# Performance work log

Hardware: AMD Instinct MI355X
Metric: run time of the kernel (lower is better)

## Reference

```python
import jax, jax.numpy as jnp
import numpy as np

B, T, DMODEL = 2, 2048, 1024
H, DK, DV = 16, 64, 64
FF = 4096
EPS = 1e-5


def _layernorm_2d(x):
    # torch LayerNorm(normalized_shape=(T, dmodel)): normalize jointly over last two
    # dims, biased variance, weight=1 / bias=0 (freshly constructed each forward).
    mu = jnp.mean(x, axis=(1, 2), keepdims=True)
    var = jnp.mean((x - mu) ** 2, axis=(1, 2), keepdims=True)
    return (x - mu) / jnp.sqrt(var + EPS)


def setup_inputs() -> dict:
    key = jax.random.key(0)
    ks = jax.random.split(key, 9)
    s = 0.02  # small init for numerical sanity (original uses uniform(-1,1))
    return {
        "x": jax.random.normal(ks[0], (B, T, DMODEL), jnp.float32),
        "Wq": jax.random.normal(ks[1], (H, DMODEL, DK), jnp.float32) * s,
        "Wk": jax.random.normal(ks[2], (H, DMODEL, DK), jnp.float32) * s,
        "Wv": jax.random.normal(ks[3], (H, DMODEL, DV), jnp.float32) * s,
        "Wo": jax.random.normal(ks[4], (DMODEL, DMODEL), jnp.float32) * s,
        "W1": jax.random.normal(ks[5], (DMODEL, FF), jnp.float32) * s,
        "b1": jnp.zeros((FF,), jnp.float32),
        "W2": jax.random.normal(ks[6], (FF, DMODEL), jnp.float32) * s,
        "b2": jnp.zeros((DMODEL,), jnp.float32),
    }


def reference(x, Wq, Wk, Wv, Wo, W1, b1, W2, b2):
    b, t, d = x.shape
    h, _, dk = Wq.shape
    dv = Wv.shape[-1]
    # per-head projections: (B,H,T,dk/dv)
    Qp = jnp.einsum("btd,hdk->bhtk", x, Wq)
    Kp = jnp.einsum("btd,hdk->bhtk", x, Wk)
    Vp = jnp.einsum("btd,hdv->bhtv", x, Wv)
    scores = jnp.einsum("bhqk,bhsk->bhqs", Qp, Kp) / np.sqrt(dk).astype(np.float32)
    # NOTE: original does torch.softmax(heads, 2) -> softmax over the QUERY axis
    attn = jax.nn.softmax(scores, axis=2)
    heads = jnp.einsum("bhqs,bhsv->bqhv", attn, Vp).reshape(b, t, h * dv)
    att_out = heads @ Wo
    o1 = _layernorm_2d(x + att_out)
    ff = jnp.maximum(o1 @ W1 + b1, 0.0) @ W2 + b2
    return _layernorm_2d(o1 + ff)
```

## Files before the change

### kernel.cpp

```cpp
#include <hip/hip_runtime.h>
#include <hip/hip_bf16.h>
#include <cstddef>
#include <cstdint>

typedef __hip_bfloat16 hbf;
typedef __attribute__((ext_vector_type(8))) __bf16 bf16x8;
typedef __attribute__((ext_vector_type(4))) float f32x4;

#define B_ 2
#define T_ 2048
#define D_ 1024
#define H_ 16
#define FF_ 4096
#define EPS_ 1e-5f
#define SCALE_ 0.125f

__device__ __forceinline__ float bf2f(hbf v) { return __bfloat162float(v); }
__device__ __forceinline__ float ldin(const void* p, size_t i, int isbf) {
  return isbf ? __bfloat162float(((const hbf*)p)[i]) : ((const float*)p)[i];
}
__device__ __forceinline__ void ston(void* p, size_t i, float v, int isbf) {
  if (isbf) ((hbf*)p)[i] = __float2bfloat16(v);
  else ((float*)p)[i] = v;
}
__device__ __forceinline__ f32x4 mfma16(bf16x8 a, bf16x8 b, f32x4 c) {
  return __builtin_amdgcn_mfma_f32_16x16x32_bf16(a, b, c, 0, 0, 0);
}
__device__ __forceinline__ bf16x8 ldfrag(const hbf* p) {
  return *(const bf16x8*)p;
}
__device__ __forceinline__ void glds16(const hbf* g, hbf* l) {
  __builtin_amdgcn_global_load_lds(
      (const __attribute__((address_space(1))) void*)g,
      (__attribute__((address_space(3))) void*)l, 16, 0, 0);
}

__global__ __launch_bounds__(256) void detect_dtype(const unsigned* x,
                                                    int* flag) {
  __shared__ int cnt[256];
  int c = 0;
  for (int i = threadIdx.x; i < 4096; i += 256) {
    unsigned low = x[i] & 0xFFFFu;
    unsigned e = (low >> 7) & 0xFFu;
    if (e >= 100u && e <= 142u) c++;
  }
  cnt[threadIdx.x] = c;
  __syncthreads();
  for (int off = 128; off > 0; off >>= 1) {
    if ((int)threadIdx.x < off) cnt[threadIdx.x] += cnt[threadIdx.x + off];
    __syncthreads();
  }
  if (threadIdx.x == 0) *flag = (cnt[0] > 2458) ? 1 : 0;
}

__global__ __launch_bounds__(256) void cvt_copy(const void* __restrict__ src,
                                                hbf* __restrict__ dst, size_t n,
                                                const int* __restrict__ flag) {
  const int f = *flag;
  for (size_t i = (size_t)blockIdx.x * 256 + threadIdx.x; i < n;
       i += (size_t)gridDim.x * 256) {
    dst[i] = __float2bfloat16(ldin(src, i, f));
  }
}

__global__ __launch_bounds__(256) void tr_k(const void* __restrict__ src,
                                            hbf* __restrict__ dst, int R, int C,
                                            const int* __restrict__ flag) {
  __shared__ float tile[32][33];
  const int f = *flag;
  const int z = blockIdx.z;
  const int c0 = blockIdx.x * 32, r0 = blockIdx.y * 32;
  const int tx = threadIdx.x & 31, ty = threadIdx.x >> 5;
  const size_t base = (size_t)z * R * C;
#pragma unroll
  for (int p = 0; p < 4; p++) {
    int rr = p * 8 + ty;
    tile[rr][tx] = ldin(src, base + (size_t)(r0 + rr) * C + c0 + tx, f);
  }
  __syncthreads();
#pragma unroll
  for (int p = 0; p < 4; p++) {
    int cc = p * 8 + ty;
    dst[base + (size_t)(c0 + cc) * R + r0 + tx] = __float2bfloat16(tile[tx][cc]);
  }
}

__global__ __launch_bounds__(256) void vt_k(const hbf* __restrict__ V,
                                            const float* __restrict__ coladj,
                                            hbf* __restrict__ Vt) {
  __shared__ hbf tile[64][72];
  const int bh = blockIdx.y;
  const int t0 = blockIdx.x * 64;
  const int tid = threadIdx.x;
  const hbf* Vb = V + (size_t)bh * T_ * 64;
  const float* adjb = coladj + (size_t)bh * T_;
  hbf* Vtb = Vt + (size_t)bh * 64 * T_;
#pragma unroll
  for (int c = 0; c < 2; c++) {
    int e = (c * 256 + tid) * 8;
    int r = e >> 6, col = e & 63;
    union alignas(16) {
      hbf h[8];
      float4 f4;
    } u;
    u.f4 = *(const float4*)(&Vb[(size_t)(t0 + r) * 64 + col]);
    float sc = __expf(-adjb[t0 + r]);
#pragma unroll
    for (int k2 = 0; k2 < 8; k2++)
      u.h[k2] = __float2bfloat16(bf2f(u.h[k2]) * sc);
    *(float4*)(&tile[r][col]) = u.f4;
  }
  __syncthreads();
#pragma unroll
  for (int c = 0; c < 2; c++) {
    int e = (c * 256 + tid) * 8;
    int v = e >> 6, tt = e & 63;
    union alignas(16) {
      hbf h[8];
      float4 f4;
    } u;
#pragma unroll
    for (int k2 = 0; k2 < 8; k2++) u.h[k2] = tile[tt + k2][v];
    *(float4*)(&Vtb[(size_t)v * T_ + t0 + tt]) = u.f4;
  }
}

template <int MODE, int BM, int BN>
__global__ __launch_bounds__(256) void gemm_bt(
    const hbf* __restrict__ A, const hbf* __restrict__ Bt, hbf* __restrict__ C,
    const hbf* __restrict__ e1, const hbf* __restrict__ e2, int M, int N,
    int K) {
  constexpr int WM = BM / 2, WN = BN / 2;
  constexpr int IF = WM / 16, JF = WN / 16;
  __shared__ alignas(16) hbf As[BM * 64];
  __shared__ alignas(16) hbf Bs[BN * 64];
  const int tid = threadIdx.x;
  const int wave = tid >> 6, lane = tid & 63;
  const int quad = lane >> 4, l16 = lane & 15;
  const int m0 = blockIdx.y * BM, n0 = blockIdx.x * BN;
  const int mw = (wave >> 1) * WM, nw = (wave & 1) * WN;
  const int srow = tid >> 3;
  const int scol = (tid & 7) * 8;
  const f32x4 zero = {0.f, 0.f, 0.f, 0.f};
  f32x4 acc[IF][JF];
#pragma unroll
  for (int i = 0; i < IF; i++)
#pragma unroll
    for (int j = 0; j < JF; j++) acc[i][j] = zero;

  const hbf* ga = &A[(size_t)(m0 + srow) * K + scol];
  const hbf* gb = &Bt[(size_t)(n0 + srow) * K + scol];
  hbf* lA = &As[wave * 512];
  hbf* lB = &Bs[wave * 512];

  for (int k0 = 0; k0 < K; k0 += 64) {
#pragma unroll
    for (int c = 0; c < BM / 32; c++)
      glds16(ga + (size_t)(c * 32) * K + k0, lA + c * 2048);
#pragma unroll
    for (int c = 0; c < BN / 32; c++)
      glds16(gb + (size_t)(c * 32) * K + k0, lB + c * 2048);
    __syncthreads();
    bf16x8 af[2][IF], bfr[2][JF];
#pragma unroll
    for (int h = 0; h < 2; h++) {
#pragma unroll
      for (int i = 0; i < IF; i++)
        af[h][i] = ldfrag(&As[(mw + i * 16 + l16) * 64 + h * 32 + quad * 8]);
#pragma unroll
      for (int j = 0; j < JF; j++)
        bfr[h][j] = ldfrag(&Bs[(nw + j * 16 + l16) * 64 + h * 32 + quad * 8]);
    }
#pragma unroll
    for (int h = 0; h < 2; h++)
#pragma unroll
      for (int i = 0; i < IF; i++)
#pragma unroll
        for (int j = 0; j < JF; j++)
          acc[i][j] = mfma16(af[h][i], bfr[h][j], acc[i][j]);
    __syncthreads();
  }
#pragma unroll
  for (int i = 0; i < IF; i++)
#pragma unroll
    for (int j = 0; j < JF; j++)
#pragma unroll
      for (int r = 0; r < 4; r++) {
        int m = m0 + mw + i * 16 + quad * 4 + r;
        int n = n0 + nw + j * 16 + l16;
        float v = acc[i][j][r];
        if (MODE == 0) {
          int which = n >> 10, n1 = n & 1023;
          int h = n1 >> 6, cc = n1 & 63;
          int b = m >> 11, t = m & (T_ - 1);
          if (which == 0) v *= SCALE_;
          C[(size_t)which * ((size_t)B_ * H_ * T_ * 64) +
            (((size_t)(b * H_ + h)) * T_ + t) * 64 + cc] = __float2bfloat16(v);
        } else if (MODE == 1) {
          C[(size_t)m * N + n] =
              __float2bfloat16(v + bf2f(e1[(size_t)m * N + n]));
        } else if (MODE == 2) {
          C[(size_t)m * N + n] = __float2bfloat16(fmaxf(v + bf2f(e1[n]), 0.f));
        } else {
          C[(size_t)m * N + n] = __float2bfloat16(v + bf2f(e1[n]) +
                                                  bf2f(e2[(size_t)m * N + n]));
        }
      }
}

__global__ __launch_bounds__(256) void attn_stats(const hbf* __restrict__ Q,
                                                  const hbf* __restrict__ K,
                                                  float* __restrict__ coladj) {
  __shared__ alignas(16) hbf Ks[64 * 72];
  __shared__ alignas(16) hbf Qs[64 * 72];
  const int bh = blockIdx.y;
  const int s0 = blockIdx.x * 64;
  const int tid = threadIdx.x;
  const int wave = tid >> 6, lane = tid & 63;
  const int quad = lane >> 4, l16 = lane & 15;
  const int sw = wave * 16;
  const hbf* Kb = K + (size_t)bh * T_ * 64;
  const hbf* Qb = Q + (size_t)bh * T_ * 64;
  const int r_ = tid >> 3, c_ = (tid & 7) * 8;
#pragma unroll
  for (int c = 0; c < 2; c++) {
    int row = c * 32 + r_;
    *(float4*)(&Ks[row * 72 + c_]) =
        *(const float4*)(&Kb[(size_t)(s0 + row) * 64 + c_]);
  }
  __syncthreads();
  bf16x8 kf0 = ldfrag(&Ks[(sw + l16) * 72 + quad * 8]);
  bf16x8 kf1 = ldfrag(&Ks[(sw + l16) * 72 + 32 + quad * 8]);
  float m_thr[4], l_thr[4];
#pragma unroll
  for (int r = 0; r < 4; r++) {
    m_thr[r] = -1e30f;
    l_thr[r] = 0.f;
  }
  const f32x4 zero = {0.f, 0.f, 0.f, 0.f};
  for (int qt = 0; qt < T_ / 64; qt++) {
    if (qt) __syncthreads();
#pragma unroll
    for (int c = 0; c < 2; c++) {
      int row = c * 32 + r_;
      *(float4*)(&Qs[row * 72 + c_]) =
          *(const float4*)(&Qb[(size_t)(qt * 64 + row) * 64 + c_]);
    }
    __syncthreads();
    f32x4 acc[4];
#pragma unroll
    for (int j = 0; j < 4; j++) {
      bf16x8 qf0 = ldfrag(&Qs[(j * 16 + l16) * 72 + quad * 8]);
      bf16x8 qf1 = ldfrag(&Qs[(j * 16 + l16) * 72 + 32 + quad * 8]);
      f32x4 a = zero;
      a = mfma16(kf0, qf0, a);
      a = mfma16(kf1, qf1, a);
      acc[j] = a;
    }
#pragma unroll
    for (int r = 0; r < 4; r++) {
      float mt = fmaxf(fmaxf(acc[0][r], acc[1][r]),
                       fmaxf(acc[2][r], acc[3][r]));
      float nm = fmaxf(m_thr[r], mt);
      float s = l_thr[r] * __expf(m_thr[r] - nm);
#pragma unroll
      for (int j = 0; j < 4; j++) s += __expf(acc[j][r] - nm);
      l_thr[r] = s;
      m_thr[r] = nm;
    }
  }
#pragma unroll
  for (int d = 1; d < 16; d <<= 1) {
#pragma unroll
    for (int r = 0; r < 4; r++) {
      float om = __shfl_xor(m_thr[r], d);
      float ol = __shfl_xor(l_thr[r], d);
      float nm = fmaxf(m_thr[r], om);
      l_thr[r] = l_thr[r] * __expf(m_thr[r] - nm) + ol * __expf(om - nm);
      m_thr[r] = nm;
    }
  }
  if (l16 == 0) {
#pragma unroll
    for (int r = 0; r < 4; r++) {
      int s = s0 + sw + quad * 4 + r;
      coladj[(size_t)bh * T_ + s] = m_thr[r] + __logf(l_thr[r]);
    }
  }
}

__global__ __launch_bounds__(256) void attn_apply(const hbf* __restrict__ Q,
                                                  const hbf* __restrict__ K,
                                                  const hbf* __restrict__ Vt,
                                                  hbf* __restrict__ heads) {
  __shared__ alignas(16) hbf Ks[64 * 72];
  __shared__ alignas(16) hbf Vs[64 * 72];
  __shared__ alignas(16) hbf Ps[4 * 32 * 72];
  const int bh = blockIdx.y;
  const int b = bh >> 4, h = bh & 15;
  const int q0 = blockIdx.x * 128;
  const int tid = threadIdx.x;
  const int wave = tid >> 6, lane = tid & 63;
  const int quad = lane >> 4, l16 = lane & 15;
  const int qw = wave * 32;
  const hbf* Qb = Q + (size_t)bh * T_ * 64;
  const hbf* Kb = K + (size_t)bh * T_ * 64;
  const hbf* Vtb = Vt + (size_t)bh * 64 * T_;
  hbf* Pw = &Ps[wave * 32 * 72];
  const int r_ = tid >> 3, c_ = (tid & 7) * 8;
  bf16x8 qf[2][2];
#pragma unroll
  for (int i = 0; i < 2; i++)
#pragma unroll
    for (int hh = 0; hh < 2; hh++)
      qf[i][hh] = *(const bf16x8*)&Qb[(size_t)(q0 + qw + i * 16 + l16) * 64 +
                                      hh * 32 + quad * 8];
  const f32x4 zero = {0.f, 0.f, 0.f, 0.f};
  f32x4 accO[2][4];
#pragma unroll
  for (int i = 0; i < 2; i++)
#pragma unroll
    for (int j = 0; j < 4; j++) accO[i][j] = zero;

  for (int st = 0; st < T_ / 64; st++) {
    if (st) __syncthreads();
#pragma unroll
    for (int c = 0; c < 2; c++) {
      int row = c * 32 + r_;
      *(float4*)(&Ks[row * 72 + c_]) =
          *(const float4*)(&Kb[(size_t)(st * 64 + row) * 64 + c_]);
      *(float4*)(&Vs[row * 72 + c_]) =
          *(const float4*)(&Vtb[(size_t)row * T_ + st * 64 + c_]);
    }
    __syncthreads();
    f32x4 accS[2][4];
#pragma unroll
    for (int j = 0; j < 4; j++) {
      bf16x8 kf0 = ldfrag(&Ks[(j * 16 + l16) * 72 + quad * 8]);
      bf16x8 kf1 = ldfrag(&Ks[(j * 16 + l16) * 72 + 32 + quad * 8]);
#pragma unroll
      for (int i = 0; i < 2; i++) {
        f32x4 a = zero;
        a = mfma16(qf[i][0], kf0, a);
        a = mfma16(qf[i][1], kf1, a);
        accS[i][j] = a;
      }
    }
#pragma unroll
    for (int j = 0; j < 4; j++) {
#pragma unroll
      for (int i = 0; i < 2; i++)
#pragma unroll
        for (int r = 0; r < 4; r++) {
          float p = __expf(accS[i][j][r]);
          Pw[(i * 16 + quad * 4 + r) * 72 + j * 16 + l16] =
              __float2bfloat16(p);
        }
    }
    bf16x8 pf[2][2];
#pragma unroll
    for (int i = 0; i < 2; i++) {
      pf[i][0] = ldfrag(&Pw[(i * 16 + l16) * 72 + quad * 8]);
      pf[i][1] = ldfrag(&Pw[(i * 16 + l16) * 72 + 32 + quad * 8]);
    }
#pragma unroll
    for (int j2 = 0; j2 < 4; j2++) {
      bf16x8 vf0 = ldfrag(&Vs[(j2 * 16 + l16) * 72 + quad * 8]);
      bf16x8 vf1 = ldfrag(&Vs[(j2 * 16 + l16) * 72 + 32 + quad * 8]);
#pragma unroll
      for (int i = 0; i < 2; i++) {
        accO[i][j2] = mfma16(pf[i][0], vf0, accO[i][j2]);
        accO[i][j2] = mfma16(pf[i][1], vf1, accO[i][j2]);
      }
    }
  }
#pragma unroll
  for (int i = 0; i < 2; i++)
#pragma unroll
    for (int j2 = 0; j2 < 4; j2++)
#pragma unroll
      for (int r = 0; r < 4; r++) {
        int q = q0 + qw + i * 16 + quad * 4 + r;
        int v = j2 * 16 + l16;
        heads[((size_t)(b * T_ + q)) * D_ + h * 64 + v] =
            __float2bfloat16(accO[i][j2][r]);
      }
}

__global__ __launch_bounds__(256) void ln_part(const hbf* __restrict__ src,
                                               float* __restrict__ red) {
  __shared__ float s1[256], s2[256];
  const int b = blockIdx.y;
  const hbf* p = src + (size_t)b * (T_ * D_);
  float sum = 0.f, sq = 0.f;
  for (size_t i = (size_t)blockIdx.x * 256 + threadIdx.x; i < (size_t)T_ * D_;
       i += (size_t)gridDim.x * 256) {
    float v = bf2f(p[i]);
    sum += v;
    sq += v * v;
  }
  s1[threadIdx.x] = sum;
  s2[threadIdx.x] = sq;
  __syncthreads();
  for (int off = 128; off > 0; off >>= 1) {
    if ((int)threadIdx.x < off) {
      s1[threadIdx.x] += s1[threadIdx.x + off];
      s2[threadIdx.x] += s2[threadIdx.x + off];
    }
    __syncthreads();
  }
  if (threadIdx.x == 0) {
    atomicAdd(&red[b * 2 + 0], s1[0]);
    atomicAdd(&red[b * 2 + 1], s2[0]);
  }
}

__global__ __launch_bounds__(256) void ln_norm(const hbf* __restrict__ src,
                                               const float* __restrict__ red,
                                               void* dst,
                                               const int* __restrict__ flag,
                                               int force_bf) {
  const int isbf = force_bf ? 1 : *flag;
  const float invN = 1.f / (float)(T_ * D_);
  for (size_t i = (size_t)blockIdx.x * 256 + threadIdx.x;
       i < (size_t)B_ * T_ * D_; i += (size_t)gridDim.x * 256) {
    int b = (int)(i >> 21);
    float mu = red[b * 2 + 0] * invN;
    float var = red[b * 2 + 1] * invN - mu * mu;
    ston(dst, i, (bf2f(src[i]) - mu) * rsqrtf(var + EPS_), isbf);
  }
}

extern "C" void kernel_launch(void* const* d_in, const int* in_sizes, int n_in,
                              void* d_out, int out_size, void* d_ws,
                              size_t ws_size, hipStream_t stream) {
  const void* x = d_in[0];
  const void* Wq = d_in[1];
  const void* Wk = d_in[2];
  const void* Wv = d_in[3];
  const void* Wo = d_in[4];
  const void* W1 = d_in[5];
  const void* b1 = d_in[6];
  const void* W2 = d_in[7];
  const void* b2 = d_in[8];

  const size_t MB = 1024 * 1024;
  if (ws_size < 89 * MB) return;

  char* w = (char*)d_ws;
  hbf* xb = (hbf*)(w + 0 * MB);
  hbf* wqkvt = (hbf*)(w + 8 * MB);
  hbf* wot = (hbf*)(w + 14 * MB);
  hbf* w1t = (hbf*)(w + 16 * MB);
  hbf* w2t = (hbf*)(w + 24 * MB);
  hbf* Qb = (hbf*)(w + 32 * MB);
  hbf* Kb = (hbf*)(w + 40 * MB);
  hbf* Vb = (hbf*)(w + 48 * MB);
  hbf* Vtb = (hbf*)(w + 56 * MB);
  hbf* heads = (hbf*)(w + 64 * MB);
  hbf* r1 = (hbf*)(w + 72 * MB);
  hbf* o1 = (hbf*)(w + 80 * MB);
  hbf* ff1 = (hbf*)(w + 32 * MB);
  float* coladj = (float*)(w + 88 * MB);
  hbf* b1b = (hbf*)(coladj + (size_t)B_ * H_ * T_);
  hbf* b2b = b1b + FF_;
  float* red = (float*)(b2b + D_);
  int* flag = (int*)(red + 8);

  hipMemsetAsync(red, 0, 8 * sizeof(float) + sizeof(int), stream);
  detect_dtype<<<1, 256, 0, stream>>>((const unsigned*)x, flag);

  const int M = B_ * T_;
  cvt_copy<<<1024, 256, 0, stream>>>(x, xb, (size_t)M * D_, flag);
  cvt_copy<<<16, 256, 0, stream>>>(b1, b1b, FF_, flag);
  cvt_copy<<<4, 256, 0, stream>>>(b2, b2b, D_, flag);
  tr_k<<<dim3(2, 32, 16), 256, 0, stream>>>(Wq, wqkvt, D_, 64, flag);
  tr_k<<<dim3(2, 32, 16), 256, 0, stream>>>(Wk, wqkvt + (size_t)D_ * D_, D_,
                                            64, flag);
  tr_k<<<dim3(2, 32, 16), 256, 0, stream>>>(Wv, wqkvt + (size_t)2 * D_ * D_,
                                            D_, 64, flag);
  tr_k<<<dim3(32, 32, 1), 256, 0, stream>>>(Wo, wot, D_, D_, flag);
  tr_k<<<dim3(128, 32, 1), 256, 0, stream>>>(W1, w1t, D_, FF_, flag);
  tr_k<<<dim3(32, 128, 1), 256, 0, stream>>>(W2, w2t, FF_, D_, flag);
  gemm_bt<0, 128, 128><<<dim3(24, 32), 256, 0, stream>>>(
      xb, wqkvt, Qb, nullptr, nullptr, M, 3 * D_, D_);
  attn_stats<<<dim3(32, 32), 256, 0, stream>>>(Qb, Kb, coladj);
  vt_k<<<dim3(32, 32), 256, 0, stream>>>(Vb, coladj, Vtb);
  attn_apply<<<dim3(16, 32), 256, 0, stream>>>(Qb, Kb, Vtb, heads);
  gemm_bt<1, 128, 64><<<dim3(16, 32), 256, 0, stream>>>(heads, wot, r1, xb,
                                                        nullptr, M, D_, D_);
  ln_part<<<dim3(256, B_), 256, 0, stream>>>(r1, red);
  ln_norm<<<4096, 256, 0, stream>>>(r1, red, o1, flag, 1);
  gemm_bt<2, 128, 128><<<dim3(32, 32), 256, 0, stream>>>(o1, w1t, ff1, b1b,
                                                         nullptr, M, FF_, D_);
  gemm_bt<3, 128, 64><<<dim3(16, 32), 256, 0, stream>>>(ff1, w2t, r1, b2b, o1,
                                                        M, D_, FF_);
  ln_part<<<dim3(256, B_), 256, 0, stream>>>(r1, red + 4);
  ln_norm<<<4096, 256, 0, stream>>>(r1, red + 4, d_out, flag, 0);
}
```

Measured before the change: 513.3 us.

## Merge prep kernels, fuse LN stats and V transpose, split-K FFN2

Combines all weight/input conversions into one launch and fuses the V scaling/transpose into attn_stats through shared memory. Computes the first LayerNorm statistics in the Wo GEMM epilogue with block reductions and atomics, removing a separate pass. The second FFN GEMM is split along K into two fp32 partial buffers, and bias plus residual are folded into the final LN stats and norm kernels. This trades fewer launches and passes for extra fp32 partial-sum traffic and workspace aliasing.

```diff
diff --git a/kernel.cpp b/kernel.cpp
--- a/kernel.cpp
+++ b/kernel.cpp
@@ -53,83 +53,73 @@
   if (threadIdx.x == 0) *flag = (cnt[0] > 2458) ? 1 : 0;
 }
 
-__global__ __launch_bounds__(256) void cvt_copy(const void* __restrict__ src,
-                                                hbf* __restrict__ dst, size_t n,
-                                                const int* __restrict__ flag) {
-  const int f = *flag;
-  for (size_t i = (size_t)blockIdx.x * 256 + threadIdx.x; i < n;
-       i += (size_t)gridDim.x * 256) {
-    dst[i] = __float2bfloat16(ldin(src, i, f));
-  }
-}
-
-__global__ __launch_bounds__(256) void tr_k(const void* __restrict__ src,
-                                            hbf* __restrict__ dst, int R, int C,
-                                            const int* __restrict__ flag) {
+__device__ __forceinline__ void tr_tile(const void* __restrict__ src,
+                                        hbf* __restrict__ dst, int R, int C,
+                                        size_t zoff, int cx, int ry, int f,
+                                        float (*tile)[33]) {
+  const int tx = threadIdx.x & 31, ty = threadIdx.x >> 5;
+  const int c0 = cx * 32, r0 = ry * 32;
+#pragma unroll
+  for (int p = 0; p < 4; p++) {
+    int rr = p * 8 + ty;
+    tile[rr][tx] = ldin(src, zoff + (size_t)(r0 + rr) * C + c0 + tx, f);
+  }
+  __syncthreads();
+#pragma unroll
+  for (int p = 0; p < 4; p++) {
+    int cc = p * 8 + ty;
+    dst[zoff + (size_t)(c0 + cc) * R + r0 + tx] = __float2bfloat16(tile[tx][cc]);
+  }
+}
+
+__global__ __launch_bounds__(256) void preconv(
+    const void* __restrict__ x, const void* __restrict__ Wq,
+    const void* __restrict__ Wk, const void* __restrict__ Wv,
+    const void* __restrict__ Wo, const void* __restrict__ W1,
+    const void* __restrict__ W2, const void* __restrict__ b1,
+    const void* __restrict__ b2, hbf* __restrict__ xb,
+    hbf* __restrict__ wqkvt, hbf* __restrict__ wot, hbf* __restrict__ w1t,
+    hbf* __restrict__ w2t, hbf* __restrict__ b1b, hbf* __restrict__ b2b,
+    const int* __restrict__ flag) {
   __shared__ float tile[32][33];
   const int f = *flag;
-  const int z = blockIdx.z;
-  const int c0 = blockIdx.x * 32, r0 = blockIdx.y * 32;
-  const int tx = threadIdx.x & 31, ty = threadIdx.x >> 5;
-  const size_t base = (size_t)z * R * C;
-#pragma unroll
-  for (int p = 0; p < 4; p++) {
-    int rr = p * 8 + ty;
-    tile[rr][tx] = ldin(src, base + (size_t)(r0 + rr) * C + c0 + tx, f);
-  }
-  __syncthreads();
-#pragma unroll
-  for (int p = 0; p < 4; p++) {
-    int cc = p * 8 + ty;
-    dst[base + (size_t)(c0 + cc) * R + r0 + tx] = __float2bfloat16(tile[tx][cc]);
-  }
-}
-
-__global__ __launch_bounds__(256) void vt_k(const hbf* __restrict__ V,
-                                            const float* __restrict__ coladj,
-                                            hbf* __restrict__ Vt) {
-  __shared__ hbf tile[64][72];
-  const int bh = blockIdx.y;
-  const int t0 = blockIdx.x * 64;
-  const int tid = threadIdx.x;
-  const hbf* Vb = V + (size_t)bh * T_ * 64;
-  const float* adjb = coladj + (size_t)bh * T_;
-  hbf* Vtb = Vt + (size_t)bh * 64 * T_;
-#pragma unroll
-  for (int c = 0; c < 2; c++) {
-    int e = (c * 256 + tid) * 8;
-    int r = e >> 6, col = e & 63;
-    union alignas(16) {
-      hbf h[8];
-      float4 f4;
-    } u;
-    u.f4 = *(const float4*)(&Vb[(size_t)(t0 + r) * 64 + col]);
-    float sc = __expf(-adjb[t0 + r]);
-#pragma unroll
-    for (int k2 = 0; k2 < 8; k2++)
-      u.h[k2] = __float2bfloat16(bf2f(u.h[k2]) * sc);
-    *(float4*)(&tile[r][col]) = u.f4;
-  }
-  __syncthreads();
-#pragma unroll
-  for (int c = 0; c < 2; c++) {
-    int e = (c * 256 + tid) * 8;
-    int v = e >> 6, tt = e & 63;
-    union alignas(16) {
-      hbf h[8];
-      float4 f4;
-    } u;
-#pragma unroll
-    for (int k2 = 0; k2 < 8; k2++) u.h[k2] = tile[tt + k2][v];
-    *(float4*)(&Vtb[(size_t)v * T_ + t0 + tt]) = u.f4;
+  const int bid = blockIdx.x;
+  if (bid < 3072) {
+    int which = bid >> 10;
+    int r = bid & 1023;
+    int z = r >> 6, rem = r & 63;
+    int ry = rem >> 1, cx = rem & 1;
+    const void* src = (which == 0) ? Wq : (which == 1) ? Wk : Wv;
+    hbf* dst = wqkvt + (size_t)which * (D_ * D_);
+    tr_tile(src, dst, 1024, 64, (size_t)z * 65536, cx, ry, f, tile);
+  } else if (bid < 4096) {
+    int t = bid - 3072;
+    tr_tile(Wo, wot, 1024, 1024, 0, t & 31, t >> 5, f, tile);
+  } else if (bid < 8192) {
+    int t = bid - 4096;
+    tr_tile(W1, w1t, 1024, 4096, 0, t & 127, t >> 7, f, tile);
+  } else if (bid < 12288) {
+    int t = bid - 8192;
+    tr_tile(W2, w2t, 4096, 1024, 0, t & 31, t >> 5, f, tile);
+  } else if (bid < 13312) {
+    size_t base = (size_t)(bid - 12288) * 4096;
+    for (int i = threadIdx.x; i < 4096; i += 256)
+      xb[base + i] = __float2bfloat16(ldin(x, base + i, f));
+  } else if (bid == 13312) {
+    for (int i = threadIdx.x; i < FF_; i += 256)
+      b1b[i] = __float2bfloat16(ldin(b1, i, f));
+  } else {
+    for (int i = threadIdx.x; i < D_; i += 256)
+      b2b[i] = __float2bfloat16(ldin(b2, i, f));
   }
 }
 
 template <int MODE, int BM, int BN>
 __global__ __launch_bounds__(256) void gemm_bt(
     const hbf* __restrict__ A, const hbf* __restrict__ Bt, hbf* __restrict__ C,
-    const hbf* __restrict__ e1, const hbf* __restrict__ e2, int M, int N,
-    int K) {
+    float* __restrict__ Cf0, float* __restrict__ Cf1,
+    const hbf* __restrict__ e1, float* __restrict__ red, int M, int N, int K,
+    int LDK) {
   constexpr int WM = BM / 2, WN = BN / 2;
   constexpr int IF = WM / 16, JF = WN / 16;
   __shared__ alignas(16) hbf As[BM * 64];
@@ -141,6 +131,7 @@
   const int mw = (wave >> 1) * WM, nw = (wave & 1) * WN;
   const int srow = tid >> 3;
   const int scol = (tid & 7) * 8;
+  const int kbase = (MODE == 4) ? blockIdx.z * K : 0;
   const f32x4 zero = {0.f, 0.f, 0.f, 0.f};
   f32x4 acc[IF][JF];
 #pragma unroll
@@ -148,18 +139,18 @@
 #pragma unroll
     for (int j = 0; j < JF; j++) acc[i][j] = zero;
 
-  const hbf* ga = &A[(size_t)(m0 + srow) * K + scol];
-  const hbf* gb = &Bt[(size_t)(n0 + srow) * K + scol];
+  const hbf* ga = &A[(size_t)(m0 + srow) * LDK + kbase + scol];
+  const hbf* gb = &Bt[(size_t)(n0 + srow) * LDK + kbase + scol];
   hbf* lA = &As[wave * 512];
   hbf* lB = &Bs[wave * 512];
 
   for (int k0 = 0; k0 < K; k0 += 64) {
 #pragma unroll
     for (int c = 0; c < BM / 32; c++)
-      glds16(ga + (size_t)(c * 32) * K + k0, lA + c * 2048);
+      glds16(ga + (size_t)(c * 32) * LDK + k0, lA + c * 2048);
 #pragma unroll
     for (int c = 0; c < BN / 32; c++)
-      glds16(gb + (size_t)(c * 32) * K + k0, lB + c * 2048);
+      glds16(gb + (size_t)(c * 32) * LDK + k0, lB + c * 2048);
     __syncthreads();
     bf16x8 af[2][IF], bfr[2][JF];
 #pragma unroll
@@ -180,6 +171,7 @@
           acc[i][j] = mfma16(af[h][i], bfr[h][j], acc[i][j]);
     __syncthreads();
   }
+  float ssum = 0.f, ssq = 0.f;
 #pragma unroll
   for (int i = 0; i < IF; i++)
 #pragma unroll
@@ -197,22 +189,45 @@
           C[(size_t)which * ((size_t)B_ * H_ * T_ * 64) +
             (((size_t)(b * H_ + h)) * T_ + t) * 64 + cc] = __float2bfloat16(v);
         } else if (MODE == 1) {
-          C[(size_t)m * N + n] =
-              __float2bfloat16(v + bf2f(e1[(size_t)m * N + n]));
+          hbf hv = __float2bfloat16(v + bf2f(e1[(size_t)m * N + n]));
+          C[(size_t)m * N + n] = hv;
+          float fv = bf2f(hv);
+          ssum += fv;
+          ssq += fv * fv;
         } else if (MODE == 2) {
           C[(size_t)m * N + n] = __float2bfloat16(fmaxf(v + bf2f(e1[n]), 0.f));
-        } else {
-          C[(size_t)m * N + n] = __float2bfloat16(v + bf2f(e1[n]) +
-                                                  bf2f(e2[(size_t)m * N + n]));
+        } else if (MODE == 4) {
+          float* Cf = blockIdx.z ? Cf1 : Cf0;
+          Cf[(size_t)m * N + n] = v;
         }
       }
+  if (MODE == 1) {
+    float* sc = (float*)As;
+    sc[tid] = ssum;
+    sc[256 + tid] = ssq;
+    __syncthreads();
+    for (int off = 128; off > 0; off >>= 1) {
+      if (tid < off) {
+        sc[tid] += sc[tid + off];
+        sc[256 + tid] += sc[256 + tid + off];
+      }
+      __syncthreads();
+    }
+    if (tid == 0) {
+      int b = m0 >> 11;
+      atomicAdd(&red[b * 2 + 0], sc[0]);
+      atomicAdd(&red[b * 2 + 1], sc[256]);
+    }
+  }
 }
 
 __global__ __launch_bounds__(256) void attn_stats(const hbf* __restrict__ Q,
                                                   const hbf* __restrict__ K,
-                                                  float* __restrict__ coladj) {
+                                                  const hbf* __restrict__ V,
+                                                  hbf* __restrict__ Vt) {
   __shared__ alignas(16) hbf Ks[64 * 72];
   __shared__ alignas(16) hbf Qs[64 * 72];
+  __shared__ float sAdj[64];
   const int bh = blockIdx.y;
   const int s0 = blockIdx.x * 64;
   const int tid = threadIdx.x;
@@ -221,6 +236,8 @@
   const int sw = wave * 16;
   const hbf* Kb = K + (size_t)bh * T_ * 64;
   const hbf* Qb = Q + (size_t)bh * T_ * 64;
+  const hbf* Vb = V + (size_t)bh * T_ * 64;
+  hbf* Vtb = Vt + (size_t)bh * 64 * T_;
   const int r_ = tid >> 3, c_ = (tid & 7) * 8;
 #pragma unroll
   for (int c = 0; c < 2; c++) {
@@ -282,10 +299,37 @@
   }
   if (l16 == 0) {
 #pragma unroll
-    for (int r = 0; r < 4; r++) {
-      int s = s0 + sw + quad * 4 + r;
-      coladj[(size_t)bh * T_ + s] = m_thr[r] + __logf(l_thr[r]);
-    }
+    for (int r = 0; r < 4; r++)
+      sAdj[sw + quad * 4 + r] = m_thr[r] + __logf(l_thr[r]);
+  }
+  __syncthreads();
+#pragma unroll
+  for (int c = 0; c < 2; c++) {
+    int e = (c * 256 + tid) * 8;
+    int r = e >> 6, col = e & 63;
+    union alignas(16) {
+      hbf h[8];
+      float4 f4;
+    } u;
+    u.f4 = *(const float4*)(&Vb[(size_t)(s0 + r) * 64 + col]);
+    float sc = __expf(-sAdj[r]);
+#pragma unroll
+    for (int k2 = 0; k2 < 8; k2++)
+      u.h[k2] = __float2bfloat16(bf2f(u.h[k2]) * sc);
+    *(float4*)(&Ks[r * 72 + col]) = u.f4;
+  }
+  __syncthreads();
+#pragma unroll
+  for (int c = 0; c < 2; c++) {
+    int e = (c * 256 + tid) * 8;
+    int v = e >> 6, tt = e & 63;
+    union alignas(16) {
+      hbf h[8];
+      float4 f4;
+    } u;
+#pragma unroll
+    for (int k2 = 0; k2 < 8; k2++) u.h[k2] = Ks[(tt + k2) * 72 + v];
+    *(float4*)(&Vtb[(size_t)v * T_ + s0 + tt]) = u.f4;
   }
 }
 
@@ -387,34 +431,6 @@
       }
 }
 
-__global__ __launch_bounds__(256) void ln_part(const hbf* __restrict__ src,
-                                               float* __restrict__ red) {
-  __shared__ float s1[256], s2[256];
-  const int b = blockIdx.y;
-  const hbf* p = src + (size_t)b * (T_ * D_);
-  float sum = 0.f, sq = 0.f;
-  for (size_t i = (size_t)blockIdx.x * 256 + threadIdx.x; i < (size_t)T_ * D_;
-       i += (size_t)gridDim.x * 256) {
-    float v = bf2f(p[i]);
-    sum += v;
-    sq += v * v;
-  }
-  s1[threadIdx.x] = sum;
-  s2[threadIdx.x] = sq;
-  __syncthreads();
-  for (int off = 128; off > 0; off >>= 1) {
-    if ((int)threadIdx.x < off) {
-      s1[threadIdx.x] += s1[threadIdx.x + off];
-      s2[threadIdx.x] += s2[threadIdx.x + off];
-    }
-    __syncthreads();
-  }
-  if (threadIdx.x == 0) {
-    atomicAdd(&red[b * 2 + 0], s1[0]);
-    atomicAdd(&red[b * 2 + 1], s2[0]);
-  }
-}
-
 __global__ __launch_bounds__(256) void ln_norm(const hbf* __restrict__ src,
                                                const float* __restrict__ red,
                                                void* dst,
@@ -431,6 +447,54 @@
   }
 }
 
+__global__ __launch_bounds__(256) void ln2_stats(const float* __restrict__ P0,
+                                                 const float* __restrict__ P1,
+                                                 const hbf* __restrict__ o1,
+                                                 const hbf* __restrict__ b2b,
+                                                 float* __restrict__ red) {
+  __shared__ float s1[256], s2[256];
+  const int b = blockIdx.y;
+  const size_t base = (size_t)b * (T_ * D_);
+  float sum = 0.f, sq = 0.f;
+  for (size_t i = (size_t)blockIdx.x * 256 + threadIdx.x; i < (size_t)T_ * D_;
+       i += (size_t)gridDim.x * 256) {
+    size_t e = base + i;
+    float v = P0[e] + P1[e] + bf2f(b2b[i & (D_ - 1)]) + bf2f(o1[e]);
+    sum += v;
+    sq += v * v;
+  }
+  s1[threadIdx.x] = sum;
+  s2[threadIdx.x] = sq;
+  __syncthreads();
+  for (int off = 128; off > 0; off >>= 1) {
+    if ((int)threadIdx.x < off) {
+      s1[threadIdx.x] += s1[threadIdx.x + off];
+      s2[threadIdx.x] += s2[threadIdx.x + off];
+    }
+    __syncthreads();
+  }
+  if (threadIdx.x == 0) {
+    atomicAdd(&red[b * 2 + 0], s1[0]);
+    atomicAdd(&red[b * 2 + 1], s2[0]);
+  }
+}
+
+__global__ __launch_bounds__(256) void ln2_norm(
+    const float* __restrict__ P0, const float* __restrict__ P1,
+    const hbf* __restrict__ o1, const hbf* __restrict__ b2b,
+    const float* __restrict__ red, void* dst, const int* __restrict__ flag) {
+  const int isbf = *flag;
+  const float invN = 1.f / (float)(T_ * D_);
+  for (size_t i = (size_t)blockIdx.x * 256 + threadIdx.x;
+       i < (size_t)B_ * T_ * D_; i += (size_t)gridDim.x * 256) {
+    int b = (int)(i >> 21);
+    float mu = red[b * 2 + 0] * invN;
+    float var = red[b * 2 + 1] * invN - mu * mu;
+    float v = P0[i] + P1[i] + bf2f(b2b[i & (D_ - 1)]) + bf2f(o1[i]);
+    ston(dst, i, (v - mu) * rsqrtf(var + EPS_), isbf);
+  }
+}
+
 extern "C" void kernel_launch(void* const* d_in, const int* in_sizes, int n_in,
                               void* d_out, int out_size, void* d_ws,
                               size_t ws_size, hipStream_t stream) {
@@ -440,8 +504,8 @@
   const void* Wv = d_in[3];
   const void* Wo = d_in[4];
   const void* W1 = d_in[5];
+  const void* W2 = d_in[7];
   const void* b1 = d_in[6];
-  const void* W2 = d_in[7];
   const void* b2 = d_in[8];
 
   const size_t MB = 1024 * 1024;
@@ -461,8 +525,9 @@
   hbf* r1 = (hbf*)(w + 72 * MB);
   hbf* o1 = (hbf*)(w + 80 * MB);
   hbf* ff1 = (hbf*)(w + 32 * MB);
-  float* coladj = (float*)(w + 88 * MB);
-  hbf* b1b = (hbf*)(coladj + (size_t)B_ * H_ * T_);
+  float* P0 = (float*)(w + 0 * MB);
+  float* P1 = (float*)(w + 64 * MB);
+  hbf* b1b = (hbf*)(w + 88 * MB);
   hbf* b2b = b1b + FF_;
   float* red = (float*)(b2b + D_);
   int* flag = (int*)(red + 8);
@@ -471,30 +536,19 @@
   detect_dtype<<<1, 256, 0, stream>>>((const unsigned*)x, flag);
 
   const int M = B_ * T_;
-  cvt_copy<<<1024, 256, 0, stream>>>(x, xb, (size_t)M * D_, flag);
-  cvt_copy<<<16, 256, 0, stream>>>(b1, b1b, FF_, flag);
-  cvt_copy<<<4, 256, 0, stream>>>(b2, b2b, D_, flag);
-  tr_k<<<dim3(2, 32, 16), 256, 0, stream>>>(Wq, wqkvt, D_, 64, flag);
-  tr_k<<<dim3(2, 32, 16), 256, 0, stream>>>(Wk, wqkvt + (size_t)D_ * D_, D_,
-                                            64, flag);
-  tr_k<<<dim3(2, 32, 16), 256, 0, stream>>>(Wv, wqkvt + (size_t)2 * D_ * D_,
-                                            D_, 64, flag);
-  tr_k<<<dim3(32, 32, 1), 256, 0, stream>>>(Wo, wot, D_, D_, flag);
-  tr_k<<<dim3(128, 32, 1), 256, 0, stream>>>(W1, w1t, D_, FF_, flag);
-  tr_k<<<dim3(32, 128, 1), 256, 0, stream>>>(W2, w2t, FF_, D_, flag);
+  preconv<<<13314, 256, 0, stream>>>(x, Wq, Wk, Wv, Wo, W1, W2, b1, b2, xb,
+                                     wqkvt, wot, w1t, w2t, b1b, b2b, flag);
   gemm_bt<0, 128, 128><<<dim3(24, 32), 256, 0, stream>>>(
-      xb, wqkvt, Qb, nullptr, nullptr, M, 3 * D_, D_);
-  attn_stats<<<dim3(32, 32), 256, 0, stream>>>(Qb, Kb, coladj);
-  vt_k<<<dim3(32, 32), 256, 0, stream>>>(Vb, coladj, Vtb);
+      xb, wqkvt, Qb, nullptr, nullptr, nullptr, nullptr, M, 3 * D_, D_, D_);
+  attn_stats<<<dim3(32, 32), 256, 0, stream>>>(Qb, Kb, Vb, Vtb);
   attn_apply<<<dim3(16, 32), 256, 0, stream>>>(Qb, Kb, Vtb, heads);
-  gemm_bt<1, 128, 64><<<dim3(16, 32), 256, 0, stream>>>(heads, wot, r1, xb,
-                                                        nullptr, M, D_, D_);
-  ln_part<<<dim3(256, B_), 256, 0, stream>>>(r1, red);
+  gemm_bt<1, 128, 64><<<dim3(16, 32), 256, 0, stream>>>(
+      heads, wot, r1, nullptr, nullptr, xb, red, M, D_, D_, D_);
   ln_norm<<<4096, 256, 0, stream>>>(r1, red, o1, flag, 1);
-  gemm_bt<2, 128, 128><<<dim3(32, 32), 256, 0, stream>>>(o1, w1t, ff1, b1b,
-                                                         nullptr, M, FF_, D_);
-  gemm_bt<3, 128, 64><<<dim3(16, 32), 256, 0, stream>>>(ff1, w2t, r1, b2b, o1,
-                                                        M, D_, FF_);
-  ln_part<<<dim3(256, B_), 256, 0, stream>>>(r1, red + 4);
-  ln_norm<<<4096, 256, 0, stream>>>(r1, red + 4, d_out, flag, 0);
-}
+  gemm_bt<2, 128, 128><<<dim3(32, 32), 256, 0, stream>>>(
+      o1, w1t, ff1, nullptr, nullptr, b1b, nullptr, M, FF_, D_, D_);
+  gemm_bt<4, 128, 128><<<dim3(8, 32, 2), 256, 0, stream>>>(
+      ff1, w2t, nullptr, P0, P1, nullptr, nullptr, M, D_, FF_ / 2, FF_);
+  ln2_stats<<<dim3(256, B_), 256, 0, stream>>>(P0, P1, o1, b2b, red + 4);
+  ln2_norm<<<2048, 256, 0, stream>>>(P0, P1, o1, b2b, red + 4, d_out, flag);
+}
```

Measured after the change: 475.7 us. 1.08x faster.
